# Optimization experiments

Measured on AMD Instinct MI355X. Metric: run time of the kernel, lower is better.

Reference implementation:

```python
import jax, jax.numpy as jnp
import numpy as np

LRELU_SLOPE = 0.2
ACT_GAIN = float(np.sqrt(2.0))  # def_gain of lrelu in StyleGAN2
CLAMP = 256.0


def _affine(w, W, b):
    # StyleGAN2 FullyConnectedLayer: runtime weight gain 1/sqrt(in_features)
    return w @ W.T * (1.0 / np.sqrt(W.shape[1])) + b[None, :]


def _gather(x, fn, pad):
    # zero rows for padding faces appended at the end, then neighborhood gather
    padded = jnp.concatenate([x, jnp.zeros((pad, x.shape[1]), x.dtype)], axis=0)
    return padded[fn]  # [N, K, C]


def _mod_texture_conv(g, styles, wc, wsd, wcr):
    # g: [N, 9, I] gathered neighborhoods; styles: [B, I]
    B, I = styles.shape
    N = g.shape[0]
    F = N // B
    # position-typed 1x1 weights: [self, 4 sides, 4 corners] -> [O, I, 9]
    W = jnp.concatenate([wc[:, :, None],
                         jnp.repeat(wsd[:, :, None], 4, axis=2),
                         jnp.repeat(wcr[:, :, None], 4, axis=2)], axis=2)
    wmod = W[None] * styles[:, None, :, None]                    # [B,O,I,9] modulate
    d = jax.lax.rsqrt(jnp.sum(wmod * wmod, axis=(2, 3)) + 1e-8)  # [B,O] demodulate
    wmod = wmod * d[:, :, None, None]
    out = jnp.einsum('bfki,boik->bfok', g.reshape(B, F, 9, I), wmod)
    return out.max(axis=3).reshape(N, -1)  # MaxPool2d((1,9)) aggregation


def _smooth_upsample(x, pool_map, fn, pad):
    # replicate coarse face features to fine faces, then smooth over 9-neighborhood
    return _gather(x[pool_map], fn, pad).mean(axis=1)


def _act(x, bias):
    # clamp_gain(lrelu(x+b), act_gain*gain, 256*gain) with gain=1
    return jnp.clip(jax.nn.leaky_relu(x + bias[None, :], LRELU_SLOPE) * ACT_GAIN, -CLAMP, CLAMP)


def setup_inputs() -> dict:
    key = jax.random.key(0)
    ks = iter(jax.random.split(key, 40))
    B, Fc, Ff = 1, 32768, 131072
    IN, OUT, GEO, COL, WD = 128, 128, 32, 3, 512
    OC1 = OUT - GEO  # 96
    PAD0, PAD1 = 1024, 4096
    nk = lambda *s: jax.random.normal(next(ks), s, jnp.float32)
    ri = lambda shape, hi: jax.random.randint(next(ks), shape, 0, hi, jnp.int32).astype(jnp.int64)
    return dict(
        x=nk(B * Fc, IN - GEO), shape_feat=nk(B * Fc, GEO), img=nk(B * Fc, COL),
        ws=nk(B, 3, WD),
        fn0=ri((B * Fc, 9), B * Fc + PAD0), fn1=ri((B * Ff, 9), B * Ff + PAD1),
        pool_map0=ri((B * Ff,), B * Fc),
        pad0=PAD0, pad1=PAD1,
        affine0_w=nk(IN, WD), affine0_b=jnp.ones((IN,), jnp.float32),
        w_center0=nk(OUT, IN), w_side0=nk(OUT, IN), w_corner0=nk(OUT, IN),
        noise_strength0=nk(1) * 0.1, bias0=nk(OUT) * 0.1, noise_const0=nk(Ff),
        affine1_w=nk(OUT, WD), affine1_b=jnp.ones((OUT,), jnp.float32),
        w_center1=nk(OC1, OUT), w_side1=nk(OC1, OUT), w_corner1=nk(OC1, OUT),
        noise_strength1=nk(1) * 0.1, bias1=nk(OC1) * 0.1, noise_const1=nk(Ff),
        affine2_w=nk(OC1, WD), affine2_b=jnp.ones((OC1,), jnp.float32),
        w_rgb=nk(COL, OC1), bias_rgb=nk(COL) * 0.1,
    )


def reference(x, shape_feat, img, ws, fn0, fn1, pool_map0, pad0, pad1,
              affine0_w, affine0_b, w_center0, w_side0, w_corner0,
              noise_strength0, bias0, noise_const0,
              affine1_w, affine1_b, w_center1, w_side1, w_corner1,
              noise_strength1, bias1, noise_const1,
              affine2_w, affine2_b, w_rgb, bias_rgb):
    B = ws.shape[0]
    h = jnp.concatenate([x, shape_feat], axis=1)  # [B*Fc, IN]
    # ---- conv0: coarse-level modulated face conv, then SmoothUpsample to fine ----
    s0 = _affine(ws[:, 0], affine0_w, affine0_b)
    h = _mod_texture_conv(_gather(h, fn0, pad0), s0, w_center0, w_side0, w_corner0)
    h = _smooth_upsample(h, pool_map0, fn1, pad1)  # [B*Ff, OUT]
    h = h + jnp.tile(noise_const0[None, :], (B, 1)).reshape(-1, 1) * noise_strength0
    h = _act(h, bias0)
    # ---- conv1: fine-level modulated face conv ----
    s1 = _affine(ws[:, 1], affine1_w, affine1_b)
    h = _mod_texture_conv(_gather(h, fn1, pad1), s1, w_center1, w_side1, w_corner1)
    h = h + jnp.tile(noise_const1[None, :], (B, 1)).reshape(-1, 1) * noise_strength1
    h = _act(h, bias1)  # [B*Ff, 96]
    # ---- torgb: 1x1 modulated conv (demodulate=False), weight_gain on styles ----
    s2 = _affine(ws[:, 2], affine2_w, affine2_b) * (1.0 / np.sqrt(w_rgb.shape[1]))
    xg = _gather(h, fn1[:, :1], pad1)[:, 0]  # kernel_size^2 == 1 -> self gather
    y = jnp.einsum('bfi,oi,bi->bfo', xg.reshape(B, -1, xg.shape[1]), w_rgb, s2)
    y = jnp.clip(y.reshape(xg.shape[0], -1) + bias_rgb[None, :], -CLAMP, CLAMP)
    img_out = _smooth_upsample(img, pool_map0, fn1, pad1) + y
    return h, img_out
```

## Files before the change

kernel.cpp:

```cpp
#include <hip/hip_runtime.h>

#define FC 32768
#define FF 131072
#define LRELU_SLOPE 0.2f
#define ACT_GAIN 1.4142135623730951f
#define CLAMP_V 256.0f

typedef __bf16 bf16x8 __attribute__((ext_vector_type(8)));
typedef float f32x4 __attribute__((ext_vector_type(4)));
typedef float f32x2 __attribute__((ext_vector_type(2)));
typedef unsigned u32x4 __attribute__((ext_vector_type(4)));
typedef unsigned short u16x4 __attribute__((ext_vector_type(4)));

static __device__ __forceinline__ unsigned short f2bf(float f) {
    unsigned u = __float_as_uint(f);
    u += 0x7FFFu + ((u >> 16) & 1u);
    return (unsigned short)(u >> 16);
}
static __device__ __forceinline__ float bf2f(unsigned short u) {
    return __uint_as_float(((unsigned)u) << 16);
}
static __device__ __forceinline__ float actf(float v) {
    v = (v < 0.f) ? v * LRELU_SLOPE : v;
    v *= ACT_GAIN;
    return fminf(fmaxf(v, -CLAMP_V), CLAMP_V);
}

__global__ void k_prep2(const float* __restrict__ wsvec,
                        const float* __restrict__ a0w, const float* __restrict__ a0b,
                        const float* __restrict__ a1w, const float* __restrict__ a1b,
                        const float* __restrict__ a2w, const float* __restrict__ a2b,
                        float* __restrict__ s0, float* __restrict__ s1, float* __restrict__ s2,
                        unsigned* __restrict__ zrow)
{
    int lane = threadIdx.x & 63;
    int t = blockIdx.x * 4 + (threadIdx.x >> 6);
    if (t >= 352) {
        if (t == 352) zrow[lane] = 0u;
        return;
    }
    int level, o;
    const float *W, *bptr; float* out;
    if (t < 128)       { level = 0; o = t;       W = a0w; bptr = a0b; out = s0; }
    else if (t < 256)  { level = 1; o = t - 128; W = a1w; bptr = a1b; out = s1; }
    else               { level = 2; o = t - 256; W = a2w; bptr = a2b; out = s2; }
    const float* wrow = wsvec + level * 512;
    const float* Wr = W + (size_t)o * 512;
    f32x4 wa = *(const f32x4*)(wrow + lane * 8);
    f32x4 wb = *(const f32x4*)(wrow + lane * 8 + 4);
    f32x4 va = *(const f32x4*)(Wr + lane * 8);
    f32x4 vb = *(const f32x4*)(Wr + lane * 8 + 4);
    float acc = wa.x * va.x + wa.y * va.y + wa.z * va.z + wa.w * va.w
              + wb.x * vb.x + wb.y * vb.y + wb.z * vb.z + wb.w * vb.w;
    #pragma unroll
    for (int off = 32; off; off >>= 1) acc += __shfl_down(acc, off, 64);
    if (lane == 0) {
        float v = acc * 0.04419417382415922f + bptr[o];
        if (level == 2) v *= 0.10206207261596577f;
        out[o] = v;
    }
}

__global__ void k_misc(const float* __restrict__ x, const float* __restrict__ sf,
                       u16x4* __restrict__ xcat,
                       const int* __restrict__ fn1, const int* __restrict__ pmap,
                       int* __restrict__ cidx)
{
    int b = blockIdx.x;
    if (b < FC * 32 / 256) {
        int gid = b * 256 + threadIdx.x;
        int f = gid >> 5;
        int c4 = (gid & 31) * 4;
        f32x4 v;
        if (c4 < 96) v = *(const f32x4*)(x + (size_t)f * 96 + c4);
        else         v = *(const f32x4*)(sf + (size_t)f * 32 + (c4 - 96));
        u16x4 o;
        o.x = f2bf(v.x); o.y = f2bf(v.y); o.z = f2bf(v.z); o.w = f2bf(v.w);
        xcat[gid] = o;
    } else {
        int gid = (b - FC * 32 / 256) * 256 + threadIdx.x;
        int g = fn1[gid];
        cidx[gid] = ((unsigned)g < FF) ? pmap[g] : -1;
    }
}

__global__ void k_wmod(const float* __restrict__ wc0, const float* __restrict__ wsd0,
                       const float* __restrict__ wcr0, const float* __restrict__ s0,
                       unsigned short* __restrict__ wm0,
                       const float* __restrict__ wc1, const float* __restrict__ wsd1,
                       const float* __restrict__ wcr1, const float* __restrict__ s1,
                       unsigned short* __restrict__ wm1,
                       const float* __restrict__ wrgb, const float* __restrict__ s2,
                       float* __restrict__ wrgbmod)
{
    int b = blockIdx.x;
    int i = threadIdx.x;
    if (b == 224) {
        for (int t = i; t < 288; t += 128) {
            int c = t / 96, k = t % 96;
            wrgbmod[c * 96 + k] = wrgb[c * 96 + k] * s2[k];
        }
        return;
    }
    const float *wc, *wsd, *wcr, *s; unsigned short* out; int o, O;
    if (b < 128) { wc = wc0; wsd = wsd0; wcr = wcr0; s = s0; out = wm0; o = b; O = 128; }
    else         { wc = wc1; wsd = wsd1; wcr = wcr1; s = s1; out = wm1; o = b - 128; O = 96; }
    float sv = s[i];
    float pc = wc[o * 128 + i] * sv;
    float ps = wsd[o * 128 + i] * sv;
    float pr = wcr[o * 128 + i] * sv;
    float part = pc * pc + 4.f * ps * ps + 4.f * pr * pr;
    __shared__ float red[2];
    #pragma unroll
    for (int off = 32; off; off >>= 1) part += __shfl_down(part, off, 64);
    if ((threadIdx.x & 63) == 0) red[threadIdx.x >> 6] = part;
    __syncthreads();
    float d = rsqrtf(red[0] + red[1] + 1e-8f);
    out[(0 * O + o) * 128 + i] = f2bf(pc * d);
    out[(1 * O + o) * 128 + i] = f2bf(ps * d);
    out[(2 * O + o) * 128 + i] = f2bf(pr * d);
}

__launch_bounds__(256, 2)
__global__ void k_gemm0(const unsigned short* __restrict__ xcat, const unsigned short* __restrict__ wm,
                        unsigned* __restrict__ y0)
{
    __shared__ unsigned short sm[4][32 * 136];
    int lane = threadIdx.x & 63;
    int w = threadIdx.x >> 6;
    int fbase = (blockIdx.x * 4 + w) * 32;
    int quad = lane >> 4, l15 = lane & 15;
    const char* hb = (const char*)xcat;
    const char* wb = (const char*)wm;
    unsigned short* lds = sm[w];

    bf16x8 a[2][4];
    #pragma unroll
    for (int mt = 0; mt < 2; ++mt)
        #pragma unroll
        for (int s = 0; s < 4; ++s)
            a[mt][s] = *(const bf16x8*)(hb + (size_t)(fbase + mt * 16 + l15) * 256 + s * 64 + quad * 16);

    for (int t = 0; t < 3; ++t) {
        bf16x8 b[8][4];
        #pragma unroll
        for (int ot = 0; ot < 8; ++ot)
            #pragma unroll
            for (int s = 0; s < 4; ++s)
                b[ot][s] = *(const bf16x8*)(wb + (size_t)(((t * 128 + ot * 16 + l15) * 128 + s * 32 + quad * 8) * 2));
        f32x4 acc[2][8];
        #pragma unroll
        for (int mt = 0; mt < 2; ++mt)
            #pragma unroll
            for (int ot = 0; ot < 8; ++ot)
                #pragma unroll
                for (int r = 0; r < 4; ++r) acc[mt][ot][r] = 0.f;
        #pragma unroll
        for (int s = 0; s < 4; ++s)
            #pragma unroll
            for (int mt = 0; mt < 2; ++mt)
                #pragma unroll
                for (int ot = 0; ot < 8; ++ot)
                    acc[mt][ot] = __builtin_amdgcn_mfma_f32_16x16x32_bf16(a[mt][s], b[ot][s], acc[mt][ot], 0, 0, 0);
        #pragma unroll
        for (int mt = 0; mt < 2; ++mt)
            #pragma unroll
            for (int ot = 0; ot < 8; ++ot)
                #pragma unroll
                for (int r = 0; r < 4; ++r)
                    lds[(mt * 16 + quad * 4 + r) * 136 + ot * 16 + l15] = f2bf(acc[mt][ot][r]);
        unsigned* yt = y0 + (size_t)t * FC * 64;
        #pragma unroll
        for (int it = 0; it < 8; ++it) {
            int ci = it * 64 + lane;
            int face = ci >> 4;
            int off = ci & 15;
            u32x4 val = *(const u32x4*)(lds + face * 136 + off * 8);
            *(u32x4*)(yt + (size_t)(fbase + face) * 64 + off * 4) = val;
        }
    }
}

__global__ void k_gather0(const unsigned* __restrict__ y0, const int* __restrict__ fn0,
                          const unsigned* __restrict__ zrow, unsigned* __restrict__ hc0)
{
    int gid = blockIdx.x * 256 + threadIdx.x;
    int g = gid >> 4;
    int c = gid & 15;
    int id[9];
    #pragma unroll
    for (int j = 0; j < 9; ++j) id[j] = fn0[g * 9 + j];
    u32x4 v[9];
    #pragma unroll
    for (int j = 0; j < 9; ++j) {
        int t = (j == 0) ? 0 : (j < 5 ? 1 : 2);
        const unsigned* p = ((unsigned)id[j] < FC) ? (y0 + (size_t)t * FC * 64 + (size_t)id[j] * 64) : zrow;
        v[j] = *(const u32x4*)(p + c * 4);
    }
    u32x4 out;
    #pragma unroll
    for (int k = 0; k < 4; ++k) {
        float m0 = bf2f((unsigned short)v[0][k]);
        float m1 = bf2f((unsigned short)(v[0][k] >> 16));
        #pragma unroll
        for (int j = 1; j < 9; ++j) {
            m0 = fmaxf(m0, bf2f((unsigned short)v[j][k]));
            m1 = fmaxf(m1, bf2f((unsigned short)(v[j][k] >> 16)));
        }
        out[k] = (unsigned)f2bf(m0) | ((unsigned)f2bf(m1) << 16);
    }
    *(u32x4*)(hc0 + (size_t)g * 64 + c * 4) = out;
}

__global__ void k_upsample(const unsigned* __restrict__ hc, const int* __restrict__ cidx,
                           const float* __restrict__ nco0,
                           const float* __restrict__ ns0p, const float* __restrict__ bias0,
                           unsigned* __restrict__ h1u, const unsigned* __restrict__ zrow)
{
    int gid = blockIdx.x * 256 + threadIdx.x;
    int f = gid >> 4;
    int c = gid & 15;
    int id[9];
    #pragma unroll
    for (int j = 0; j < 9; ++j) id[j] = cidx[f * 9 + j];
    u32x4 v[9];
    #pragma unroll
    for (int j = 0; j < 9; ++j) {
        const unsigned* p = (id[j] >= 0) ? (hc + (size_t)id[j] * 64) : zrow;
        v[j] = *(const u32x4*)(p + c * 4);
    }
    float nz = nco0[f] * ns0p[0];
    f32x4 b0 = *(const f32x4*)(bias0 + c * 8);
    f32x4 b1 = *(const f32x4*)(bias0 + c * 8 + 4);
    const float inv9 = 1.f / 9.f;
    u32x4 out;
    #pragma unroll
    for (int k = 0; k < 4; ++k) {
        float a0 = 0.f, a1 = 0.f;
        #pragma unroll
        for (int j = 0; j < 9; ++j) {
            a0 += bf2f((unsigned short)v[j][k]);
            a1 += bf2f((unsigned short)(v[j][k] >> 16));
        }
        float bb0 = (k < 2) ? ((k == 0) ? b0.x : b0.z) : ((k == 2) ? b1.x : b1.z);
        float bb1 = (k < 2) ? ((k == 0) ? b0.y : b0.w) : ((k == 2) ? b1.y : b1.w);
        a0 = actf(a0 * inv9 + nz + bb0);
        a1 = actf(a1 * inv9 + nz + bb1);
        out[k] = (unsigned)f2bf(a0) | ((unsigned)f2bf(a1) << 16);
    }
    *(u32x4*)(h1u + (size_t)f * 64 + c * 4) = out;
}

__launch_bounds__(256, 2)
__global__ void k_gemm1(const unsigned short* __restrict__ h1, const unsigned short* __restrict__ wm,
                        unsigned* __restrict__ ybase)
{
    __shared__ unsigned short sm[4][32 * 104];
    int lane = threadIdx.x & 63;
    int w = threadIdx.x >> 6;
    int fbase = (blockIdx.x * 4 + w) * 32;
    int quad = lane >> 4, l15 = lane & 15;
    const char* hb = (const char*)h1;
    const char* wb = (const char*)wm;
    unsigned short* lds = sm[w];

    bf16x8 a[2][4];
    #pragma unroll
    for (int mt = 0; mt < 2; ++mt)
        #pragma unroll
        for (int s = 0; s < 4; ++s)
            a[mt][s] = *(const bf16x8*)(hb + (size_t)(fbase + mt * 16 + l15) * 256 + s * 64 + quad * 16);

    for (int t = 0; t < 3; ++t) {
        bf16x8 b[6][4];
        #pragma unroll
        for (int ot = 0; ot < 6; ++ot)
            #pragma unroll
            for (int s = 0; s < 4; ++s)
                b[ot][s] = *(const bf16x8*)(wb + (size_t)(((t * 96 + ot * 16 + l15) * 128 + s * 32 + quad * 8) * 2));
        f32x4 acc[2][6];
        #pragma unroll
        for (int mt = 0; mt < 2; ++mt)
            #pragma unroll
            for (int ot = 0; ot < 6; ++ot)
                #pragma unroll
                for (int r = 0; r < 4; ++r) acc[mt][ot][r] = 0.f;
        #pragma unroll
        for (int s = 0; s < 4; ++s)
            #pragma unroll
            for (int mt = 0; mt < 2; ++mt)
                #pragma unroll
                for (int ot = 0; ot < 6; ++ot)
                    acc[mt][ot] = __builtin_amdgcn_mfma_f32_16x16x32_bf16(a[mt][s], b[ot][s], acc[mt][ot], 0, 0, 0);
        #pragma unroll
        for (int mt = 0; mt < 2; ++mt)
            #pragma unroll
            for (int ot = 0; ot < 6; ++ot)
                #pragma unroll
                for (int r = 0; r < 4; ++r)
                    lds[(mt * 16 + quad * 4 + r) * 104 + ot * 16 + l15] = f2bf(acc[mt][ot][r]);
        unsigned* yt = ybase + (size_t)t * FF * 48;
        #pragma unroll
        for (int it = 0; it < 6; ++it) {
            int ci = it * 64 + lane;
            int face = ci / 12;
            int off = ci - face * 12;
            u32x4 val = *(const u32x4*)(lds + face * 104 + off * 8);
            *(u32x4*)(yt + (size_t)(fbase + face) * 48 + off * 4) = val;
        }
    }
}

__global__ void k_gather1(const char* __restrict__ yb, const int* __restrict__ fn1,
                          const unsigned* __restrict__ zrow,
                          const float* __restrict__ nco1, const float* __restrict__ ns1p,
                          const float* __restrict__ bias1, float* __restrict__ hout)
{
    int gid = blockIdx.x * 256 + threadIdx.x;
    int f = gid >> 4;
    int c = gid & 15;
    if (c >= 12) return;
    int id[9];
    #pragma unroll
    for (int j = 0; j < 9; ++j) id[j] = fn1[f * 9 + j];
    u32x4 v[9];
    #pragma unroll
    for (int j = 0; j < 9; ++j) {
        int t = (j == 0) ? 0 : (j < 5 ? 1 : 2);
        const char* p = ((unsigned)id[j] < FF) ? (yb + (size_t)t * FF * 192 + (size_t)id[j] * 192) : (const char*)zrow;
        v[j] = *(const u32x4*)(p + c * 16);
    }
    float nz = nco1[f] * ns1p[0];
    f32x4 o0, o1;
    #pragma unroll
    for (int k = 0; k < 4; ++k) {
        float m0 = bf2f((unsigned short)v[0][k]);
        float m1 = bf2f((unsigned short)(v[0][k] >> 16));
        #pragma unroll
        for (int j = 1; j < 9; ++j) {
            m0 = fmaxf(m0, bf2f((unsigned short)v[j][k]));
            m1 = fmaxf(m1, bf2f((unsigned short)(v[j][k] >> 16)));
        }
        float r0 = actf(m0 + nz + bias1[c * 8 + k * 2]);
        float r1 = actf(m1 + nz + bias1[c * 8 + k * 2 + 1]);
        if (k < 2) { o0[k * 2] = r0; o0[k * 2 + 1] = r1; }
        else       { o1[(k - 2) * 2] = r0; o1[(k - 2) * 2 + 1] = r1; }
    }
    float* op = hout + (size_t)f * 96 + c * 8;
    *(f32x4*)op = o0;
    *(f32x4*)(op + 4) = o1;
}

__global__ void k_rgbdense(const float* __restrict__ h, const float* __restrict__ wrgbmod,
                           f32x4* __restrict__ rgb3)
{
    __shared__ float wsm[288];
    int t = threadIdx.x;
    if (t < 256) wsm[t] = wrgbmod[t];
    if (t < 32)  wsm[256 + t] = wrgbmod[256 + t];
    __syncthreads();
    int f = blockIdx.x * 256 + t;
    const float* hr = h + (size_t)f * 96;
    float y0 = 0.f, y1 = 0.f, y2 = 0.f;
    #pragma unroll
    for (int i4 = 0; i4 < 24; ++i4) {
        f32x4 xv = *(const f32x4*)(hr + i4 * 4);
        const float* w0 = wsm + i4 * 4;
        const float* w1 = wsm + 96 + i4 * 4;
        const float* w2 = wsm + 192 + i4 * 4;
        y0 += xv.x * w0[0] + xv.y * w0[1] + xv.z * w0[2] + xv.w * w0[3];
        y1 += xv.x * w1[0] + xv.y * w1[1] + xv.z * w1[2] + xv.w * w1[3];
        y2 += xv.x * w2[0] + xv.y * w2[1] + xv.z * w2[2] + xv.w * w2[3];
    }
    f32x4 o; o.x = y0; o.y = y1; o.z = y2; o.w = 0.f;
    rgb3[f] = o;
}

__global__ void k_torgb2(const f32x4* __restrict__ rgb3, const int* __restrict__ fn1,
                         const int* __restrict__ cidx, const float* __restrict__ img,
                         const float* __restrict__ brgb, float* __restrict__ imgout)
{
    int f = blockIdx.x * 256 + threadIdx.x;
    int g0 = fn1[(size_t)f * 9];
    float y0 = 0.f, y1 = 0.f, y2 = 0.f;
    if ((unsigned)g0 < FF) {
        f32x4 y = rgb3[g0];
        y0 = y.x; y1 = y.y; y2 = y.z;
    }
    y0 = fminf(fmaxf(y0 + brgb[0], -CLAMP_V), CLAMP_V);
    y1 = fminf(fmaxf(y1 + brgb[1], -CLAMP_V), CLAMP_V);
    y2 = fminf(fmaxf(y2 + brgb[2], -CLAMP_V), CLAMP_V);
    float i0 = 0.f, i1 = 0.f, i2 = 0.f;
    #pragma unroll
    for (int j = 0; j < 9; ++j) {
        int id = cidx[f * 9 + j];
        if (id >= 0) {
            const float* ir = img + (size_t)id * 3;
            i0 += ir[0]; i1 += ir[1]; i2 += ir[2];
        }
    }
    const float inv9 = 1.f / 9.f;
    imgout[(size_t)f * 3 + 0] = i0 * inv9 + y0;
    imgout[(size_t)f * 3 + 1] = i1 * inv9 + y1;
    imgout[(size_t)f * 3 + 2] = i2 * inv9 + y2;
}

extern "C" void kernel_launch(void* const* d_in, const int* in_sizes, int n_in,
                              void* d_out, int out_size, void* d_ws, size_t ws_size,
                              hipStream_t stream) {
    const float* x     = (const float*)d_in[0];
    const float* sfeat = (const float*)d_in[1];
    const float* img   = (const float*)d_in[2];
    const float* wsv   = (const float*)d_in[3];
    const int* fn0     = (const int*)d_in[4];
    const int* fn1     = (const int*)d_in[5];
    const int* pmap    = (const int*)d_in[6];
    const float* a0w   = (const float*)d_in[9];
    const float* a0b   = (const float*)d_in[10];
    const float* wc0   = (const float*)d_in[11];
    const float* wsd0  = (const float*)d_in[12];
    const float* wcr0  = (const float*)d_in[13];
    const float* ns0   = (const float*)d_in[14];
    const float* bias0 = (const float*)d_in[15];
    const float* nco0  = (const float*)d_in[16];
    const float* a1w   = (const float*)d_in[17];
    const float* a1b   = (const float*)d_in[18];
    const float* wc1   = (const float*)d_in[19];
    const float* wsd1  = (const float*)d_in[20];
    const float* wcr1  = (const float*)d_in[21];
    const float* ns1   = (const float*)d_in[22];
    const float* bias1 = (const float*)d_in[23];
    const float* nco1  = (const float*)d_in[24];
    const float* a2w   = (const float*)d_in[25];
    const float* a2b   = (const float*)d_in[26];
    const float* wrgb  = (const float*)d_in[27];
    const float* brgb  = (const float*)d_in[28];

    char* wsb = (char*)d_ws;
    float* s0            = (float*)(wsb + 0);
    float* s1            = (float*)(wsb + 512);
    float* s2            = (float*)(wsb + 1024);
    float* wrgbmod       = (float*)(wsb + 1536);
    unsigned* zrow       = (unsigned*)(wsb + 4096);
    unsigned short* wm0  = (unsigned short*)(wsb + 8192);
    unsigned short* wm1  = (unsigned short*)(wsb + 8192 + 98304);
    unsigned short* xcat = (unsigned short*)(wsb + 262144);
    unsigned* y0         = (unsigned*)(wsb + 8650752);
    unsigned* hc0        = (unsigned*)(wsb + 33816576);
    unsigned short* h1   = (unsigned short*)(wsb + 42205184);
    int* cidx            = (int*)(wsb + 75759616);
    unsigned* ybase      = (unsigned*)(wsb + 80478208);
    f32x4* rgb3          = (f32x4*)(wsb + 155975680);

    float* out_h   = (float*)d_out;
    float* out_img = out_h + (size_t)FF * 96;

    k_misc<<<FC * 32 / 256 + FF * 9 / 256, 256, 0, stream>>>(x, sfeat, (u16x4*)xcat, fn1, pmap, cidx);
    k_prep2<<<89, 256, 0, stream>>>(wsv, a0w, a0b, a1w, a1b, a2w, a2b, s0, s1, s2, zrow);
    k_wmod<<<225, 128, 0, stream>>>(wc0, wsd0, wcr0, s0, wm0,
                                    wc1, wsd1, wcr1, s1, wm1, wrgb, s2, wrgbmod);
    k_gemm0<<<FC / 128, 256, 0, stream>>>(xcat, wm0, y0);
    k_gather0<<<FC * 16 / 256, 256, 0, stream>>>(y0, fn0, zrow, hc0);
    k_upsample<<<FF * 16 / 256, 256, 0, stream>>>(hc0, cidx, nco0, ns0, bias0, (unsigned*)h1, zrow);
    k_gemm1<<<FF / 128, 256, 0, stream>>>(h1, wm1, ybase);
    k_gather1<<<FF * 16 / 256, 256, 0, stream>>>((const char*)ybase, fn1, zrow, nco1, ns1, bias1, out_h);
    k_rgbdense<<<FF / 256, 256, 0, stream>>>(out_h, wrgbmod, rgb3);
    k_torgb2<<<FF / 256, 256, 0, stream>>>(rgb3, fn1, cidx, img, brgb, out_img);
}
```

Measured before the change: 314.6 us.

## Split GEMMs across position types, store MFMA output directly, fuse RGB dense into gather1

```diff
diff --git a/kernel.cpp b/kernel.cpp
--- a/kernel.cpp
+++ b/kernel.cpp
@@ -10,12 +10,16 @@
 typedef float f32x4 __attribute__((ext_vector_type(4)));
 typedef float f32x2 __attribute__((ext_vector_type(2)));
 typedef unsigned u32x4 __attribute__((ext_vector_type(4)));
+typedef unsigned u32x2 __attribute__((ext_vector_type(2)));
 typedef unsigned short u16x4 __attribute__((ext_vector_type(4)));
 
 static __device__ __forceinline__ unsigned short f2bf(float f) {
     unsigned u = __float_as_uint(f);
     u += 0x7FFFu + ((u >> 16) & 1u);
     return (unsigned short)(u >> 16);
+}
+static __device__ __forceinline__ unsigned packbf(float a, float b) {
+    return (unsigned)f2bf(a) | ((unsigned)f2bf(b) << 16);
 }
 static __device__ __forceinline__ float bf2f(unsigned short u) {
     return __uint_as_float(((unsigned)u) << 16);
@@ -121,62 +125,57 @@
     out[(2 * O + o) * 128 + i] = f2bf(pr * d);
 }
 
-__launch_bounds__(256, 2)
+__launch_bounds__(256, 3)
 __global__ void k_gemm0(const unsigned short* __restrict__ xcat, const unsigned short* __restrict__ wm,
                         unsigned* __restrict__ y0)
 {
-    __shared__ unsigned short sm[4][32 * 136];
     int lane = threadIdx.x & 63;
     int w = threadIdx.x >> 6;
-    int fbase = (blockIdx.x * 4 + w) * 32;
+    int bx = blockIdx.x;
+    int t = bx % 3, chunk = bx / 3;
+    int fbase = (chunk * 4 + w) * 32;
     int quad = lane >> 4, l15 = lane & 15;
     const char* hb = (const char*)xcat;
     const char* wb = (const char*)wm;
-    unsigned short* lds = sm[w];
-
-    bf16x8 a[2][4];
-    #pragma unroll
-    for (int mt = 0; mt < 2; ++mt)
+
+    bf16x8 bfr[2][4];
+    #pragma unroll
+    for (int nt = 0; nt < 2; ++nt)
         #pragma unroll
         for (int s = 0; s < 4; ++s)
-            a[mt][s] = *(const bf16x8*)(hb + (size_t)(fbase + mt * 16 + l15) * 256 + s * 64 + quad * 16);
-
-    for (int t = 0; t < 3; ++t) {
-        bf16x8 b[8][4];
-        #pragma unroll
-        for (int ot = 0; ot < 8; ++ot)
+            bfr[nt][s] = *(const bf16x8*)(hb + (size_t)(fbase + nt * 16 + l15) * 256 + s * 64 + quad * 16);
+
+    f32x4 acc[2][8];
+    #pragma unroll
+    for (int nt = 0; nt < 2; ++nt)
+        #pragma unroll
+        for (int mt = 0; mt < 8; ++mt)
             #pragma unroll
-            for (int s = 0; s < 4; ++s)
-                b[ot][s] = *(const bf16x8*)(wb + (size_t)(((t * 128 + ot * 16 + l15) * 128 + s * 32 + quad * 8) * 2));
-        f32x4 acc[2][8];
-        #pragma unroll
-        for (int mt = 0; mt < 2; ++mt)
+            for (int r = 0; r < 4; ++r) acc[nt][mt][r] = 0.f;
+
+    #pragma unroll
+    for (int s = 0; s < 4; ++s) {
+        bf16x8 afr[8];
+        #pragma unroll
+        for (int mt = 0; mt < 8; ++mt)
+            afr[mt] = *(const bf16x8*)(wb + (size_t)(((t * 128 + mt * 16 + l15) * 128 + s * 32 + quad * 8) * 2));
+        #pragma unroll
+        for (int nt = 0; nt < 2; ++nt)
             #pragma unroll
-            for (int ot = 0; ot < 8; ++ot)
-                #pragma unroll
-                for (int r = 0; r < 4; ++r) acc[mt][ot][r] = 0.f;
-        #pragma unroll
-        for (int s = 0; s < 4; ++s)
-            #pragma unroll
-            for (int mt = 0; mt < 2; ++mt)
-                #pragma unroll
-                for (int ot = 0; ot < 8; ++ot)
-                    acc[mt][ot] = __builtin_amdgcn_mfma_f32_16x16x32_bf16(a[mt][s], b[ot][s], acc[mt][ot], 0, 0, 0);
-        #pragma unroll
-        for (int mt = 0; mt < 2; ++mt)
-            #pragma unroll
-            for (int ot = 0; ot < 8; ++ot)
-                #pragma unroll
-                for (int r = 0; r < 4; ++r)
-                    lds[(mt * 16 + quad * 4 + r) * 136 + ot * 16 + l15] = f2bf(acc[mt][ot][r]);
-        unsigned* yt = y0 + (size_t)t * FC * 64;
-        #pragma unroll
-        for (int it = 0; it < 8; ++it) {
-            int ci = it * 64 + lane;
-            int face = ci >> 4;
-            int off = ci & 15;
-            u32x4 val = *(const u32x4*)(lds + face * 136 + off * 8);
-            *(u32x4*)(yt + (size_t)(fbase + face) * 64 + off * 4) = val;
+            for (int mt = 0; mt < 8; ++mt)
+                acc[nt][mt] = __builtin_amdgcn_mfma_f32_16x16x32_bf16(afr[mt], bfr[nt][s], acc[nt][mt], 0, 0, 0);
+    }
+
+    unsigned* yt = y0 + (size_t)t * FC * 64;
+    #pragma unroll
+    for (int nt = 0; nt < 2; ++nt) {
+        int face = fbase + nt * 16 + l15;
+        #pragma unroll
+        for (int mt = 0; mt < 8; ++mt) {
+            u32x2 v;
+            v.x = packbf(acc[nt][mt][0], acc[nt][mt][1]);
+            v.y = packbf(acc[nt][mt][2], acc[nt][mt][3]);
+            *(u32x2*)(yt + (size_t)face * 64 + mt * 8 + quad * 2) = v;
         }
     }
 }
@@ -207,7 +206,7 @@
             m0 = fmaxf(m0, bf2f((unsigned short)v[j][k]));
             m1 = fmaxf(m1, bf2f((unsigned short)(v[j][k] >> 16)));
         }
-        out[k] = (unsigned)f2bf(m0) | ((unsigned)f2bf(m1) << 16);
+        out[k] = packbf(m0, m1);
     }
     *(u32x4*)(hc0 + (size_t)g * 64 + c * 4) = out;
 }
@@ -246,67 +245,62 @@
         float bb1 = (k < 2) ? ((k == 0) ? b0.y : b0.w) : ((k == 2) ? b1.y : b1.w);
         a0 = actf(a0 * inv9 + nz + bb0);
         a1 = actf(a1 * inv9 + nz + bb1);
-        out[k] = (unsigned)f2bf(a0) | ((unsigned)f2bf(a1) << 16);
+        out[k] = packbf(a0, a1);
     }
     *(u32x4*)(h1u + (size_t)f * 64 + c * 4) = out;
 }
 
-__launch_bounds__(256, 2)
+__launch_bounds__(256, 4)
 __global__ void k_gemm1(const unsigned short* __restrict__ h1, const unsigned short* __restrict__ wm,
                         unsigned* __restrict__ ybase)
 {
-    __shared__ unsigned short sm[4][32 * 104];
     int lane = threadIdx.x & 63;
     int w = threadIdx.x >> 6;
-    int fbase = (blockIdx.x * 4 + w) * 32;
+    int bx = blockIdx.x;
+    int t = bx % 3, chunk = bx / 3;
+    int fbase = (chunk * 4 + w) * 32;
     int quad = lane >> 4, l15 = lane & 15;
     const char* hb = (const char*)h1;
     const char* wb = (const char*)wm;
-    unsigned short* lds = sm[w];
-
-    bf16x8 a[2][4];
-    #pragma unroll
-    for (int mt = 0; mt < 2; ++mt)
+
+    bf16x8 bfr[2][4];
+    #pragma unroll
+    for (int nt = 0; nt < 2; ++nt)
         #pragma unroll
         for (int s = 0; s < 4; ++s)
-            a[mt][s] = *(const bf16x8*)(hb + (size_t)(fbase + mt * 16 + l15) * 256 + s * 64 + quad * 16);
-
-    for (int t = 0; t < 3; ++t) {
-        bf16x8 b[6][4];
-        #pragma unroll
-        for (int ot = 0; ot < 6; ++ot)
+            bfr[nt][s] = *(const bf16x8*)(hb + (size_t)(fbase + nt * 16 + l15) * 256 + s * 64 + quad * 16);
+
+    f32x4 acc[2][6];
+    #pragma unroll
+    for (int nt = 0; nt < 2; ++nt)
+        #pragma unroll
+        for (int mt = 0; mt < 6; ++mt)
             #pragma unroll
-            for (int s = 0; s < 4; ++s)
-                b[ot][s] = *(const bf16x8*)(wb + (size_t)(((t * 96 + ot * 16 + l15) * 128 + s * 32 + quad * 8) * 2));
-        f32x4 acc[2][6];
-        #pragma unroll
-        for (int mt = 0; mt < 2; ++mt)
+            for (int r = 0; r < 4; ++r) acc[nt][mt][r] = 0.f;
+
+    #pragma unroll
+    for (int s = 0; s < 4; ++s) {
+        bf16x8 afr[6];
+        #pragma unroll
+        for (int mt = 0; mt < 6; ++mt)
+            afr[mt] = *(const bf16x8*)(wb + (size_t)(((t * 96 + mt * 16 + l15) * 128 + s * 32 + quad * 8) * 2));
+        #pragma unroll
+        for (int nt = 0; nt < 2; ++nt)
             #pragma unroll
-            for (int ot = 0; ot < 6; ++ot)
-                #pragma unroll
-                for (int r = 0; r < 4; ++r) acc[mt][ot][r] = 0.f;
-        #pragma unroll
-        for (int s = 0; s < 4; ++s)
-            #pragma unroll
-            for (int mt = 0; mt < 2; ++mt)
-                #pragma unroll
-                for (int ot = 0; ot < 6; ++ot)
-                    acc[mt][ot] = __builtin_amdgcn_mfma_f32_16x16x32_bf16(a[mt][s], b[ot][s], acc[mt][ot], 0, 0, 0);
-        #pragma unroll
-        for (int mt = 0; mt < 2; ++mt)
-            #pragma unroll
-            for (int ot = 0; ot < 6; ++ot)
-                #pragma unroll
-                for (int r = 0; r < 4; ++r)
-                    lds[(mt * 16 + quad * 4 + r) * 104 + ot * 16 + l15] = f2bf(acc[mt][ot][r]);
-        unsigned* yt = ybase + (size_t)t * FF * 48;
-        #pragma unroll
-        for (int it = 0; it < 6; ++it) {
-            int ci = it * 64 + lane;
-            int face = ci / 12;
-            int off = ci - face * 12;
-            u32x4 val = *(const u32x4*)(lds + face * 104 + off * 8);
-            *(u32x4*)(yt + (size_t)(fbase + face) * 48 + off * 4) = val;
+            for (int mt = 0; mt < 6; ++mt)
+                acc[nt][mt] = __builtin_amdgcn_mfma_f32_16x16x32_bf16(afr[mt], bfr[nt][s], acc[nt][mt], 0, 0, 0);
+    }
+
+    unsigned* yt = ybase + (size_t)t * FF * 48;
+    #pragma unroll
+    for (int nt = 0; nt < 2; ++nt) {
+        int face = fbase + nt * 16 + l15;
+        #pragma unroll
+        for (int mt = 0; mt < 6; ++mt) {
+            u32x2 v;
+            v.x = packbf(acc[nt][mt][0], acc[nt][mt][1]);
+            v.y = packbf(acc[nt][mt][2], acc[nt][mt][3]);
+            *(u32x2*)(yt + (size_t)face * 48 + mt * 8 + quad * 2) = v;
         }
     }
 }
@@ -314,12 +308,13 @@
 __global__ void k_gather1(const char* __restrict__ yb, const int* __restrict__ fn1,
                           const unsigned* __restrict__ zrow,
                           const float* __restrict__ nco1, const float* __restrict__ ns1p,
-                          const float* __restrict__ bias1, float* __restrict__ hout)
+                          const float* __restrict__ bias1, const float* __restrict__ wrgbmod,
+                          float* __restrict__ hout, f32x4* __restrict__ rgb3)
 {
     int gid = blockIdx.x * 256 + threadIdx.x;
     int f = gid >> 4;
     int c = gid & 15;
-    if (c >= 12) return;
+    int ce = (c < 12) ? c : 11;
     int id[9];
     #pragma unroll
     for (int j = 0; j < 9; ++j) id[j] = fn1[f * 9 + j];
@@ -328,7 +323,7 @@
     for (int j = 0; j < 9; ++j) {
         int t = (j == 0) ? 0 : (j < 5 ? 1 : 2);
         const char* p = ((unsigned)id[j] < FF) ? (yb + (size_t)t * FF * 192 + (size_t)id[j] * 192) : (const char*)zrow;
-        v[j] = *(const u32x4*)(p + c * 16);
+        v[j] = *(const u32x4*)(p + ce * 16);
     }
     float nz = nco1[f] * ns1p[0];
     f32x4 o0, o1;
@@ -341,39 +336,39 @@
             m0 = fmaxf(m0, bf2f((unsigned short)v[j][k]));
             m1 = fmaxf(m1, bf2f((unsigned short)(v[j][k] >> 16)));
         }
-        float r0 = actf(m0 + nz + bias1[c * 8 + k * 2]);
-        float r1 = actf(m1 + nz + bias1[c * 8 + k * 2 + 1]);
+        float r0 = actf(m0 + nz + bias1[ce * 8 + k * 2]);
+        float r1 = actf(m1 + nz + bias1[ce * 8 + k * 2 + 1]);
         if (k < 2) { o0[k * 2] = r0; o0[k * 2 + 1] = r1; }
         else       { o1[(k - 2) * 2] = r0; o1[(k - 2) * 2 + 1] = r1; }
     }
-    float* op = hout + (size_t)f * 96 + c * 8;
-    *(f32x4*)op = o0;
-    *(f32x4*)(op + 4) = o1;
-}
-
-__global__ void k_rgbdense(const float* __restrict__ h, const float* __restrict__ wrgbmod,
-                           f32x4* __restrict__ rgb3)
-{
-    __shared__ float wsm[288];
-    int t = threadIdx.x;
-    if (t < 256) wsm[t] = wrgbmod[t];
-    if (t < 32)  wsm[256 + t] = wrgbmod[256 + t];
-    __syncthreads();
-    int f = blockIdx.x * 256 + t;
-    const float* hr = h + (size_t)f * 96;
-    float y0 = 0.f, y1 = 0.f, y2 = 0.f;
-    #pragma unroll
-    for (int i4 = 0; i4 < 24; ++i4) {
-        f32x4 xv = *(const f32x4*)(hr + i4 * 4);
-        const float* w0 = wsm + i4 * 4;
-        const float* w1 = wsm + 96 + i4 * 4;
-        const float* w2 = wsm + 192 + i4 * 4;
-        y0 += xv.x * w0[0] + xv.y * w0[1] + xv.z * w0[2] + xv.w * w0[3];
-        y1 += xv.x * w1[0] + xv.y * w1[1] + xv.z * w1[2] + xv.w * w1[3];
-        y2 += xv.x * w2[0] + xv.y * w2[1] + xv.z * w2[2] + xv.w * w2[3];
-    }
-    f32x4 o; o.x = y0; o.y = y1; o.z = y2; o.w = 0.f;
-    rgb3[f] = o;
+    float msk = (c < 12) ? 1.f : 0.f;
+    f32x4 w00 = *(const f32x4*)(wrgbmod + ce * 8);
+    f32x4 w01 = *(const f32x4*)(wrgbmod + ce * 8 + 4);
+    f32x4 w10 = *(const f32x4*)(wrgbmod + 96 + ce * 8);
+    f32x4 w11 = *(const f32x4*)(wrgbmod + 96 + ce * 8 + 4);
+    f32x4 w20 = *(const f32x4*)(wrgbmod + 192 + ce * 8);
+    f32x4 w21 = *(const f32x4*)(wrgbmod + 192 + ce * 8 + 4);
+    float p0 = msk * (o0.x * w00.x + o0.y * w00.y + o0.z * w00.z + o0.w * w00.w
+                    + o1.x * w01.x + o1.y * w01.y + o1.z * w01.z + o1.w * w01.w);
+    float p1 = msk * (o0.x * w10.x + o0.y * w10.y + o0.z * w10.z + o0.w * w10.w
+                    + o1.x * w11.x + o1.y * w11.y + o1.z * w11.z + o1.w * w11.w);
+    float p2 = msk * (o0.x * w20.x + o0.y * w20.y + o0.z * w20.z + o0.w * w20.w
+                    + o1.x * w21.x + o1.y * w21.y + o1.z * w21.z + o1.w * w21.w);
+    #pragma unroll
+    for (int off = 8; off; off >>= 1) {
+        p0 += __shfl_xor(p0, off, 16);
+        p1 += __shfl_xor(p1, off, 16);
+        p2 += __shfl_xor(p2, off, 16);
+    }
+    if (c < 12) {
+        float* op = hout + (size_t)f * 96 + c * 8;
+        *(f32x4*)op = o0;
+        *(f32x4*)(op + 4) = o1;
+    }
+    if (c == 12) {
+        f32x4 o; o.x = p0; o.y = p1; o.z = p2; o.w = 0.f;
+        rgb3[f] = o;
+    }
 }
 
 __global__ void k_torgb2(const f32x4* __restrict__ rgb3, const int* __restrict__ fn1,
@@ -459,11 +454,11 @@
     k_prep2<<<89, 256, 0, stream>>>(wsv, a0w, a0b, a1w, a1b, a2w, a2b, s0, s1, s2, zrow);
     k_wmod<<<225, 128, 0, stream>>>(wc0, wsd0, wcr0, s0, wm0,
                                     wc1, wsd1, wcr1, s1, wm1, wrgb, s2, wrgbmod);
-    k_gemm0<<<FC / 128, 256, 0, stream>>>(xcat, wm0, y0);
+    k_gemm0<<<768, 256, 0, stream>>>(xcat, wm0, y0);
     k_gather0<<<FC * 16 / 256, 256, 0, stream>>>(y0, fn0, zrow, hc0);
     k_upsample<<<FF * 16 / 256, 256, 0, stream>>>(hc0, cidx, nco0, ns0, bias0, (unsigned*)h1, zrow);
-    k_gemm1<<<FF / 128, 256, 0, stream>>>(h1, wm1, ybase);
-    k_gather1<<<FF * 16 / 256, 256, 0, stream>>>((const char*)ybase, fn1, zrow, nco1, ns1, bias1, out_h);
-    k_rgbdense<<<FF / 256, 256, 0, stream>>>(out_h, wrgbmod, rgb3);
+    k_gemm1<<<3072, 256, 0, stream>>>(h1, wm1, ybase);
+    k_gather1<<<FF * 16 / 256, 256, 0, stream>>>((const char*)ybase, fn1, zrow, nco1, ns1, bias1,
+                                                 wrgbmod, out_h, rgb3);
     k_torgb2<<<FF / 256, 256, 0, stream>>>(rgb3, fn1, cidx, img, brgb, out_img);
 }
```

Measured after the change: 312.3 us. Within noise of the previous version (-0.7%).
